# Optimization experiments

Measured on AMD Instinct MI355X. Metric: run time of the kernel, lower is better.

## Reference

```python
import jax, jax.numpy as jnp
import numpy as np

OBS_LEN = 8
N_PED = 2048      # total pedestrians
G = 64            # number of scenes (uniform size)
NP = N_PED // G   # pedestrians per scene = 32
H = 128           # action_decoder_hidden_dim == action_encoder_hidden_dim == f_in == f_out
DIN = 64          # action_encoder_input_dim
DD = 64           # distance_embedding_dim
NH = 4            # n_heads (hard-coded to 4 in GAT)


def setup_inputs() -> dict:
    key = jax.random.key(0)
    ks = jax.random.split(key, 16)
    s = 0.1  # weight scale (xavier-ish)
    starts = (jnp.arange(G) * NP).astype(jnp.int64)
    seq_start_end = jnp.stack([starts, starts + NP], axis=1)
    return {
        "obs_traj": jax.random.normal(ks[0], (OBS_LEN, N_PED, 2), jnp.float32),
        "goal_hidden_state": jax.random.normal(ks[1], (N_PED, H), jnp.float32),
        "goal": jax.random.normal(ks[2], (N_PED, 2), jnp.float32),
        "action": jax.random.normal(ks[3], (N_PED, 2), jnp.float32),
        "h0": jax.random.normal(ks[4], (N_PED, H), jnp.float32),
        "c0": jax.random.normal(ks[5], (N_PED, H), jnp.float32),
        "W_emb": jax.random.normal(ks[6], (2, DIN), jnp.float32) * s,
        "b_emb": jnp.zeros((DIN,), jnp.float32),
        "W_ih": jax.random.normal(ks[7], (4 * H, DIN), jnp.float32) * s,
        "W_hh": jax.random.normal(ks[8], (4 * H, H), jnp.float32) * s,
        "b_ih": jnp.zeros((4 * H,), jnp.float32),
        "b_hh": jnp.zeros((4 * H,), jnp.float32),
        "W_dist": jax.random.normal(ks[9], (8, DD), jnp.float32) * s,
        "b_dist": jnp.zeros((DD,), jnp.float32),
        "W_gate": jax.random.normal(ks[10], (DD, H), jnp.float32) * s,
        "b_gate": jnp.zeros((H,), jnp.float32),
        "gat_w": jax.random.normal(ks[11], (NH, 1, H, H), jnp.float32) * s,
        "gat_a": jax.random.normal(ks[12], (1, 1, 2 * H, 1), jnp.float32) * s,
        "gat_bias": jnp.zeros((H,), jnp.float32),
        "seq_start_end": seq_start_end,
    }


def _forward(obs_traj, goal_hidden_state, goal, action, h0, c0,
             W_emb, b_emb, W_ih, W_hh, b_ih, b_hh,
             W_dist, b_dist, W_gate, b_gate, gat_w, gat_a, gat_bias,
             seq_start_end):
    T, N, _ = obs_traj.shape
    g_num = seq_start_end.shape[0]
    n = N // g_num  # uniform group size

    # --- ActionEncoder: embed + LSTMCell loop over obs_len (lax.scan) ---
    x = jax.nn.relu(obs_traj.reshape(-1, 2) @ W_emb + b_emb).reshape(T, N, -1)

    def lstm_step(carry, xt):
        h, c = carry
        gates = xt @ W_ih.T + b_ih + h @ W_hh.T + b_hh  # torch gate order i,f,g,o
        i, f, g, o = jnp.split(gates, 4, axis=-1)
        c = jax.nn.sigmoid(f) * c + jax.nn.sigmoid(i) * jnp.tanh(g)
        h = jax.nn.sigmoid(o) * jnp.tanh(c)
        return (h, c), None

    (action_hidden, _), _ = jax.lax.scan(lstm_step, (h0, c0), x)  # [N, H]

    Hd = action_hidden.shape[-1]
    ahg = action_hidden.reshape(g_num, n, Hd)
    ghg = goal_hidden_state.reshape(g_num, n, Hd)
    glg = goal.reshape(g_num, n, 2)
    acg = action.reshape(g_num, n, 2)

    eye = jnp.eye(n, dtype=action_hidden.dtype)[:, :, None]  # [n, n, 1]

    def gat_group(ah, gh, gl, ac):
        # InteractionGate.cal_gate: dist[i,j] = [action_i, goal_i, action_j, goal_j]
        a_i = jnp.broadcast_to(ac[:, None, :], (n, n, 2))
        g_i = jnp.broadcast_to(gl[:, None, :], (n, n, 2))
        a_j = jnp.broadcast_to(ac[None, :, :], (n, n, 2))
        g_j = jnp.broadcast_to(gl[None, :, :], (n, n, 2))
        dist = jnp.concatenate([a_i, g_i, a_j, g_j], axis=-1)  # [n, n, 8]
        gate = jax.nn.sigmoid(jax.nn.relu(dist @ W_dist + b_dist) @ W_gate + b_gate)  # [n, n, H]

        # gate_action[i,j] = gate[i,j] * tanh(action_hidden[j])
        gate_action = gate * jnp.tanh(ah[None, :, :])
        # diagonal -> goal_hidden[i], off-diag -> gated action
        goal_action = eye * gh[None, :, :] + (1.0 - eye) * gate_action  # [n, n, H]

        h_other = jnp.concatenate([ah[:, None, :], goal_action], axis=1)  # [n, n+1, H]
        h_self = jnp.broadcast_to(ah[:, None, :], (n, n + 1, Hd))          # [n, n+1, H]

        # GraphAttentionLayer
        w = gat_w[:, 0]  # [NH, H, H]
        hs = jnp.einsum('nkf,hfo->hnko', h_self, w)   # [NH, n, n+1, H]
        ho = jnp.einsum('nkf,hfo->hnko', h_other, w)  # [NH, n, n+1, H]
        scores = jnp.concatenate([hs, ho], axis=-1) @ gat_a[0, 0, :, 0]  # [NH, n, n+1]
        alpha = jax.nn.softmax(jax.nn.leaky_relu(scores, 0.2), axis=-1)
        out = jnp.mean(jnp.sum(alpha[..., None] * ho, axis=2), axis=0)  # [n, H]
        return jax.nn.relu(out) + gat_bias

    out = jax.vmap(gat_group)(ahg, ghg, glg, acg)  # [G, n, H]
    return out.reshape(N, Hd)


def reference(obs_traj, goal_hidden_state, goal, action, h0, c0,
              W_emb, b_emb, W_ih, W_hh, b_ih, b_hh,
              W_dist, b_dist, W_gate, b_gate, gat_w, gat_a, gat_bias,
              seq_start_end):
    return _forward(obs_traj, goal_hidden_state, goal, action, h0, c0,
                    W_emb, b_emb, W_ih, W_hh, b_ih, b_hh,
                    W_dist, b_dist, W_gate, b_gate, gat_w, gat_a, gat_bias,
                    seq_start_end)
```

## Files before the change

kernel.cpp:

```cpp
#include <hip/hip_runtime.h>

#define N_PED 2048
#define NGROUP 64
#define NPG 32
#define HDIM 128
#define DIN 64
#define DDIM 64
#define NHEAD 4
#define TOBS 8

typedef __attribute__((ext_vector_type(8))) short bf16x8;
typedef __attribute__((ext_vector_type(4))) float f32x4;

__device__ __forceinline__ float sigm(float x){ return 1.f/(1.f + __expf(-x)); }
__device__ __forceinline__ float tanh_fast(float x){ return 1.f - 2.f/(__expf(2.f*x) + 1.f); }
__device__ __forceinline__ short f2bf(float f){
    unsigned u = __float_as_uint(f);
    unsigned r = (u + 0x7fffu + ((u >> 16) & 1u)) >> 16;
    return (short)r;
}
__device__ __forceinline__ float bf2f(unsigned short b){
    return __uint_as_float(((unsigned)b) << 16);
}
__device__ __forceinline__ unsigned pk2(float a, float b){
    return (unsigned)(unsigned short)f2bf(a) | ((unsigned)(unsigned short)f2bf(b) << 16);
}

#define WS_AHB   0
#define WS_TAHB  524288
#define WS_VW    1048576
#define WS_GF    1052672
#define WS_WF    1069056

__global__ __launch_bounds__(256) void prep_kernel(const float* __restrict__ gat_w,
                                                   const float* __restrict__ gat_a,
                                                   float* __restrict__ VW) {
    __shared__ float sa[2*HDIM];
    __shared__ float red[32][8][2];
    const int tid = threadIdx.x;
    if (tid < 256) sa[tid] = gat_a[tid];
    __syncthreads();
    const int rl = tid >> 3, ch = tid & 7;
    const int row = blockIdx.x*32 + rl;
    const float* rp = gat_w + (size_t)row*HDIM + ch*16;
    float v = 0.f, w1 = 0.f;
    #pragma unroll
    for (int e = 0; e < 16; ++e) {
        float wv = rp[e];
        v  += wv * sa[HDIM + ch*16 + e];
        w1 += wv * sa[ch*16 + e];
    }
    red[rl][ch][0] = v; red[rl][ch][1] = w1;
    __syncthreads();
    if (ch == 0) {
        float sv = 0.f, sw = 0.f;
        #pragma unroll
        for (int e = 0; e < 8; ++e) { sv += red[rl][e][0]; sw += red[rl][e][1]; }
        VW[row]       = sv;
        VW[512 + row] = sw;
    }
}

__global__ __launch_bounds__(512) void pack_kernel(const float* __restrict__ W_gate,
                                                   const float* __restrict__ gat_w,
                                                   unsigned char* __restrict__ ws) {
    const int id = blockIdx.x*512 + threadIdx.x;
    if (id >= 9216) return;
    uint4* Gf4 = reinterpret_cast<uint4*>(ws + WS_GF);
    uint4* Wf4 = reinterpret_cast<uint4*>(ws + WS_WF);
    if (id < 1024) {
        const int fid = id >> 6, L = id & 63;
        const int kt = fid >> 3, nt = fid & 7;
        const int q = L >> 4, ln = L & 15;
        float v[8];
        #pragma unroll
        for (int j = 0; j < 8; ++j)
            v[j] = W_gate[(size_t)(kt*32 + q*8 + j)*HDIM + nt*16 + ln];
        Gf4[id] = uint4{ pk2(v[0],v[1]), pk2(v[2],v[3]), pk2(v[4],v[5]), pk2(v[6],v[7]) };
    } else {
        const int id2 = id - 1024;
        const int fid = id2 >> 6, L = id2 & 63;
        const int kt = fid >> 3, nt = fid & 7;
        const int q = L >> 4, ln = L & 15;
        float v[8];
        #pragma unroll
        for (int j = 0; j < 8; ++j) {
            int F = kt*32 + q*8 + j;
            v[j] = gat_w[(size_t)(F >> 7)*16384 + (size_t)(F & 127)*HDIM + nt*16 + ln];
        }
        Wf4[id2] = uint4{ pk2(v[0],v[1]), pk2(v[2],v[3]), pk2(v[4],v[5]), pk2(v[6],v[7]) };
    }
}

#define KPAD 216
__global__ __launch_bounds__(512) void lstm_kernel(
    const float* __restrict__ obs, const float* __restrict__ h0,
    const float* __restrict__ c0,  const float* __restrict__ W_emb,
    const float* __restrict__ b_emb, const float* __restrict__ W_ih,
    const float* __restrict__ W_hh,  const float* __restrict__ b_ih,
    const float* __restrict__ b_hh,
    unsigned short* __restrict__ AHb, unsigned short* __restrict__ TAHb)
{
    __shared__ short Xl[16][KPAD];
    __shared__ float sEmb[192];

    const int tid  = threadIdx.x;
    const int ped0 = blockIdx.x * 16;
    const int w    = tid >> 6;
    const int lane = tid & 63;
    const int q    = lane >> 4;
    const int ln   = lane & 15;
    const int u    = w*16 + ln;

    if (tid < 192) sEmb[tid] = (tid < 128) ? W_emb[tid] : b_emb[tid - 128];

    bf16x8 bfr[4][6];
    #pragma unroll
    for (int idx = 0; idx < 4; ++idx) {
        const int n = idx*128 + u;
        #pragma unroll
        for (int kt = 0; kt < 6; ++kt) {
            const float* src = (kt < 2) ? (W_ih + (size_t)n*DIN  + kt*32 + q*8)
                                        : (W_hh + (size_t)n*HDIM + (kt-2)*32 + q*8);
            bf16x8 b;
            #pragma unroll
            for (int j = 0; j < 8; ++j) b[j] = f2bf(src[j]);
            bfr[idx][kt] = b;
        }
    }
    float bsv[4];
    #pragma unroll
    for (int idx = 0; idx < 4; ++idx) bsv[idx] = b_ih[idx*128 + u] + b_hh[idx*128 + u];

    float c_st[4];
    #pragma unroll
    for (int reg = 0; reg < 4; ++reg)
        c_st[reg] = c0[(size_t)(ped0 + q*4 + reg)*HDIM + u];

    #pragma unroll
    for (int reg = 0; reg < 4; ++reg)
        Xl[q*4 + reg][64 + u] = f2bf(h0[(size_t)(ped0 + q*4 + reg)*HDIM + u]);
    {
        const int ped = tid >> 5, d0 = (tid & 31)*2;
        const float2 ob = reinterpret_cast<const float2*>(obs)[(size_t)(ped0 + ped)];
        float x0 = fmaxf(ob.x*sEmb[d0]   + ob.y*sEmb[64+d0]   + sEmb[128+d0],   0.f);
        float x1 = fmaxf(ob.x*sEmb[d0+1] + ob.y*sEmb[64+d0+1] + sEmb[128+d0+1], 0.f);
        *reinterpret_cast<unsigned*>(&Xl[ped][d0]) = pk2(x0, x1);
    }
    __syncthreads();

    float hval[4];
    for (int t = 0; t < TOBS; ++t) {
        bf16x8 afr[6];
        #pragma unroll
        for (int kt = 0; kt < 6; ++kt)
            afr[kt] = *reinterpret_cast<const bf16x8*>(&Xl[ln][kt*32 + q*8]);

        f32x4 acc[4];
        #pragma unroll
        for (int idx = 0; idx < 4; ++idx) {
            f32x4 a = { bsv[idx], bsv[idx], bsv[idx], bsv[idx] };
            #pragma unroll
            for (int kt = 0; kt < 6; ++kt)
                a = __builtin_amdgcn_mfma_f32_16x16x32_bf16(afr[kt], bfr[idx][kt], a, 0, 0, 0);
            acc[idx] = a;
        }
        #pragma unroll
        for (int reg = 0; reg < 4; ++reg) {
            float c = sigm(acc[1][reg])*c_st[reg] + sigm(acc[0][reg])*tanh_fast(acc[2][reg]);
            c_st[reg] = c;
            hval[reg] = sigm(acc[3][reg])*tanh_fast(c);
        }
        __syncthreads();

        if (t < TOBS-1) {
            #pragma unroll
            for (int reg = 0; reg < 4; ++reg)
                Xl[q*4 + reg][64 + u] = f2bf(hval[reg]);
            {
                const int ped = tid >> 5, d0 = (tid & 31)*2;
                const float2 ob = reinterpret_cast<const float2*>(obs)[(size_t)((t+1)*N_PED + ped0 + ped)];
                float x0 = fmaxf(ob.x*sEmb[d0]   + ob.y*sEmb[64+d0]   + sEmb[128+d0],   0.f);
                float x1 = fmaxf(ob.x*sEmb[d0+1] + ob.y*sEmb[64+d0+1] + sEmb[128+d0+1], 0.f);
                *reinterpret_cast<unsigned*>(&Xl[ped][d0]) = pk2(x0, x1);
            }
            __syncthreads();
        }
    }

    #pragma unroll
    for (int reg = 0; reg < 4; ++reg) {
        const size_t off = (size_t)(ped0 + q*4 + reg)*HDIM + u;
        AHb[off]  = (unsigned short)f2bf(hval[reg]);
        TAHb[off] = (unsigned short)f2bf(tanh_fast(hval[reg]));
    }
}

__global__ __launch_bounds__(256) void gat_kernel(
    const unsigned short* __restrict__ AHb,
    const unsigned short* __restrict__ TAHb,
    const float* __restrict__ VW,
    const unsigned char* __restrict__ ws,
    const float* __restrict__ ghs,
    const float* __restrict__ goal,
    const float* __restrict__ action,
    const float* __restrict__ W_dist,
    const float* __restrict__ b_dist,
    const float* __restrict__ b_gate,
    const float* __restrict__ gat_bias,
    float* __restrict__ out)
{
    __shared__ unsigned short sGAb[80][136];
    __shared__ unsigned short sTAHb[32][136];
    __shared__ unsigned short st1b[64][72];
    __shared__ unsigned short sU[4][520];
    __shared__ float sAl[2][4][34];
    __shared__ float sPj[80][8];
    __shared__ float sWd[8][64];
    __shared__ float sbd[64];
    __shared__ float sbg[128];
    __shared__ float sgb[128];
    __shared__ float sAC[32][2], sGL[32][2];

    const int tid = threadIdx.x;
    const int g   = blockIdx.x >> 3;
    const int i0  = (blockIdx.x & 7) * 4;
    const int p0  = g * NPG;
    const int w   = tid >> 6;
    const int L   = tid & 63;
    const int q   = L >> 4;
    const int ln  = L & 15;

    const bf16x8* Gf8 = reinterpret_cast<const bf16x8*>(ws + WS_GF);
    const bf16x8* Wf8 = reinterpret_cast<const bf16x8*>(ws + WS_WF);

    for (int s = tid; s < 512; s += 256) {
        int j = s >> 4, c = s & 15;
        *reinterpret_cast<uint4*>(&sTAHb[j][c*8]) =
            *reinterpret_cast<const uint4*>(&TAHb[(size_t)(p0 + j)*HDIM + c*8]);
    }
    if (tid < 128) {
        sbg[tid] = b_gate[tid];
        sgb[tid] = gat_bias[tid];
    } else if (tid < 192) {
        sbd[tid-128] = b_dist[tid-128];
    } else {
        int j = tid - 192;
        int pd = j & 31;
        if (j < 32) { const float2 a = reinterpret_cast<const float2*>(action)[p0+pd];
                      sAC[pd][0]=a.x; sAC[pd][1]=a.y; }
        else        { const float2 gl = reinterpret_cast<const float2*>(goal)[p0+pd];
                      sGL[pd][0]=gl.x; sGL[pd][1]=gl.y; }
    }
    if (tid < 256) {
        int rr = tid >> 6, k = tid & 63;
        sWd[rr][k]   = W_dist[rr*64 + k];
        sWd[rr+4][k] = W_dist[(rr+4)*64 + k];
    }

    bf16x8 vf[4];
    #pragma unroll
    for (int kt = 0; kt < 4; ++kt) {
        bf16x8 b;
        #pragma unroll
        for (int j = 0; j < 8; ++j) {
            int k = kt*32 + q*8 + j;
            float v = 0.f;
            if (ln < 4)      v = VW[ln*HDIM + k];
            else if (ln < 8) v = VW[512 + (ln-4)*HDIM + k];
            b[j] = f2bf(v);
        }
        vf[kt] = b;
    }
    __syncthreads();

    for (int half = 0; half < 2; ++half) {
        {
            const int k = tid & 63, mg = tid >> 6;
            float base[2];
            #pragma unroll
            for (int rh = 0; rh < 2; ++rh) {
                int i = i0 + half*2 + rh;
                base[rh] = sAC[i][0]*sWd[0][k] + sAC[i][1]*sWd[1][k]
                         + sGL[i][0]*sWd[2][k] + sGL[i][1]*sWd[3][k] + sbd[k];
            }
            #pragma unroll
            for (int mm = 0; mm < 16; ++mm) {
                int m = mg*16 + mm, j = m & 31;
                float v = base[m>>5] + sAC[j][0]*sWd[4][k] + sAC[j][1]*sWd[5][k]
                                     + sGL[j][0]*sWd[6][k] + sGL[j][1]*sWd[7][k];
                st1b[m][k] = (unsigned short)f2bf(fmaxf(v, 0.f));
            }
        }
        __syncthreads();

        {
            bf16x8 afr[2];
            #pragma unroll
            for (int kt = 0; kt < 2; ++kt)
                afr[kt] = *reinterpret_cast<const bf16x8*>(&st1b[w*16 + ln][kt*32 + q*8]);
            for (int nt = 0; nt < 8; ++nt) {
                float bg = sbg[nt*16 + ln];
                f32x4 a = { bg, bg, bg, bg };
                a = __builtin_amdgcn_mfma_f32_16x16x32_bf16(afr[0], Gf8[(0*8+nt)*64 + L], a, 0, 0, 0);
                a = __builtin_amdgcn_mfma_f32_16x16x32_bf16(afr[1], Gf8[(1*8+nt)*64 + L], a, 0, 0, 0);
                #pragma unroll
                for (int reg = 0; reg < 4; ++reg) {
                    int mrow = w*16 + q*4 + reg;
                    int n = nt*16 + ln;
                    float ga = sigm(a[reg]) * bf2f(sTAHb[mrow & 31][n]);
                    sGAb[mrow][n] = (unsigned short)f2bf(ga);
                }
            }
        }
        __syncthreads();

        {
            int rh = tid >> 7, f = tid & 127;
            int irow = i0 + half*2 + rh;
            sGAb[rh*32 + irow][f] = (unsigned short)f2bf(ghs[(size_t)(p0 + irow)*HDIM + f]);
            sGAb[64 + rh][f]      = AHb[(size_t)(p0 + irow)*HDIM + f];
        }
        __syncthreads();

        {
            int nmt = (w == 0) ? 2 : 1;
            for (int e = 0; e < nmt; ++e) {
                int mt = (e == 0) ? w : 4;
                bf16x8 afr;
                f32x4 a = { 0.f, 0.f, 0.f, 0.f };
                #pragma unroll
                for (int kt = 0; kt < 4; ++kt) {
                    afr = *reinterpret_cast<const bf16x8*>(&sGAb[mt*16 + ln][kt*32 + q*8]);
                    a = __builtin_amdgcn_mfma_f32_16x16x32_bf16(afr, vf[kt], a, 0, 0, 0);
                }
                if (ln < 8) {
                    #pragma unroll
                    for (int reg = 0; reg < 4; ++reg)
                        sPj[mt*16 + q*4 + reg][ln] = a[reg];
                }
            }
        }
        __syncthreads();

        if (tid < 8) {
            int rh = tid >> 2, h = tid & 3;
            float sa_ = sPj[64 + rh][4 + h];
            float x0  = sa_ + sPj[64 + rh][h];
            x0 = (x0 < 0.f) ? 0.2f*x0 : x0;
            float sum = 1.f;
            sAl[rh][h][0] = 1.f;
            for (int k = 1; k <= 32; ++k) {
                float x = sa_ + sPj[rh*32 + k - 1][h];
                x = (x < 0.f) ? 0.2f*x : x;
                float e = __expf(x - x0);
                sAl[rh][h][k] = e; sum += e;
            }
            float inv = 1.f/sum;
            for (int k = 0; k <= 32; ++k) sAl[rh][h][k] *= inv;
        }
        __syncthreads();

        {
            int rh = w & 1, ntb = (w >> 1) * 4;
            int r  = half*2 + rh;
            bf16x8 afr;
            #pragma unroll
            for (int jj = 0; jj < 8; ++jj)
                afr[jj] = f2bf(sAl[rh][ln & 3][1 + q*8 + jj]);
            for (int t = 0; t < 4; ++t) {
                int nt = ntb + t;
                bf16x8 bfr;
                #pragma unroll
                for (int jj = 0; jj < 8; ++jj)
                    bfr[jj] = (short)sGAb[rh*32 + q*8 + jj][nt*16 + ln];
                f32x4 a = { 0.f, 0.f, 0.f, 0.f };
                a = __builtin_amdgcn_mfma_f32_16x16x32_bf16(afr, bfr, a, 0, 0, 0);
                if (L < 16) {
                    #pragma unroll
                    for (int reg = 0; reg < 4; ++reg) {
                        float uv = a[reg] + sAl[rh][reg][0] * bf2f(sGAb[64 + rh][nt*16 + ln]);
                        sU[r][reg*HDIM + nt*16 + ln] = (unsigned short)f2bf(uv);
                    }
                }
            }
        }
        __syncthreads();
    }

    {
        bf16x8 afr[16];
        #pragma unroll
        for (int kt = 0; kt < 16; ++kt)
            afr[kt] = *reinterpret_cast<const bf16x8*>(&sU[ln & 3][kt*32 + q*8]);
        for (int e = 0; e < 2; ++e) {
            int nt = w*2 + e;
            f32x4 a = { 0.f, 0.f, 0.f, 0.f };
            #pragma unroll
            for (int kt = 0; kt < 16; ++kt)
                a = __builtin_amdgcn_mfma_f32_16x16x32_bf16(afr[kt], Wf8[(kt*8+nt)*64 + L], a, 0, 0, 0);
            if (L < 16) {
                int o = nt*16 + ln;
                #pragma unroll
                for (int reg = 0; reg < 4; ++reg) {
                    float val = fmaxf(a[reg]*0.25f, 0.f) + sgb[o];
                    out[(size_t)(p0 + i0 + reg)*HDIM + o] = val;
                }
            }
        }
    }
}

extern "C" void kernel_launch(void* const* d_in, const int* in_sizes, int n_in,
                              void* d_out, int out_size, void* d_ws, size_t ws_size,
                              hipStream_t stream) {
    const float* obs      = (const float*)d_in[0];
    const float* ghs      = (const float*)d_in[1];
    const float* goal     = (const float*)d_in[2];
    const float* action   = (const float*)d_in[3];
    const float* h0       = (const float*)d_in[4];
    const float* c0       = (const float*)d_in[5];
    const float* W_emb    = (const float*)d_in[6];
    const float* b_emb    = (const float*)d_in[7];
    const float* W_ih     = (const float*)d_in[8];
    const float* W_hh     = (const float*)d_in[9];
    const float* b_ih     = (const float*)d_in[10];
    const float* b_hh     = (const float*)d_in[11];
    const float* W_dist   = (const float*)d_in[12];
    const float* b_dist   = (const float*)d_in[13];
    const float* W_gate   = (const float*)d_in[14];
    const float* b_gate   = (const float*)d_in[15];
    const float* gat_w    = (const float*)d_in[16];
    const float* gat_a    = (const float*)d_in[17];
    const float* gat_bias = (const float*)d_in[18];

    unsigned char* ws = (unsigned char*)d_ws;
    unsigned short* AHb  = (unsigned short*)(ws + WS_AHB);
    unsigned short* TAHb = (unsigned short*)(ws + WS_TAHB);
    float* VW            = (float*)(ws + WS_VW);
    float* out = (float*)d_out;

    hipLaunchKernelGGL(prep_kernel, dim3(16),  dim3(256), 0, stream, gat_w, gat_a, VW);
    hipLaunchKernelGGL(pack_kernel, dim3(18),  dim3(512), 0, stream, W_gate, gat_w, ws);
    hipLaunchKernelGGL(lstm_kernel, dim3(128), dim3(512), 0, stream,
                       obs, h0, c0, W_emb, b_emb, W_ih, W_hh, b_ih, b_hh, AHb, TAHb);
    hipLaunchKernelGGL(gat_kernel,  dim3(512), dim3(256), 0, stream,
                       AHb, TAHb, VW, ws, ghs, goal, action,
                       W_dist, b_dist, b_gate, gat_bias, out);
}
```

Measured before the change: 144.8 us.

## Fuse prep/pack kernels, halve LSTM block size, double-buffer LSTM input

Merges the prep and pack kernels into one launch to save a kernel launch. The LSTM kernel now handles 8 pedestrians per block (duplicated into the 16-row MFMA tile) over 256 blocks, so more CUs are busy. Its input tile is double-buffered, which drops one barrier per timestep. Sigmoid and tanh now use a hardware reciprocal. The cost is half of the MFMA work being redundant, and the approximate reciprocal adds a small precision risk.

Measured after the change: 137.1 us. -5.3%, faster.

```diff
diff --git a/kernel.cpp b/kernel.cpp
--- a/kernel.cpp
+++ b/kernel.cpp
@@ -12,8 +12,12 @@
 typedef __attribute__((ext_vector_type(8))) short bf16x8;
 typedef __attribute__((ext_vector_type(4))) float f32x4;
 
-__device__ __forceinline__ float sigm(float x){ return 1.f/(1.f + __expf(-x)); }
-__device__ __forceinline__ float tanh_fast(float x){ return 1.f - 2.f/(__expf(2.f*x) + 1.f); }
+__device__ __forceinline__ float sigm(float x){
+    return __builtin_amdgcn_rcpf(1.f + __expf(-x));
+}
+__device__ __forceinline__ float tanh_fast(float x){
+    return 1.f - 2.f*__builtin_amdgcn_rcpf(__expf(2.f*x) + 1.f);
+}
 __device__ __forceinline__ short f2bf(float f){
     unsigned u = __float_as_uint(f);
     unsigned r = (u + 0x7fffu + ((u >> 16) & 1u)) >> 16;
@@ -32,63 +36,65 @@
 #define WS_GF    1052672
 #define WS_WF    1069056
 
-__global__ __launch_bounds__(256) void prep_kernel(const float* __restrict__ gat_w,
-                                                   const float* __restrict__ gat_a,
-                                                   float* __restrict__ VW) {
-    __shared__ float sa[2*HDIM];
-    __shared__ float red[32][8][2];
+__global__ __launch_bounds__(512) void prep_pack_kernel(
+    const float* __restrict__ gat_w, const float* __restrict__ gat_a,
+    const float* __restrict__ W_gate, unsigned char* __restrict__ ws)
+{
     const int tid = threadIdx.x;
-    if (tid < 256) sa[tid] = gat_a[tid];
-    __syncthreads();
-    const int rl = tid >> 3, ch = tid & 7;
-    const int row = blockIdx.x*32 + rl;
-    const float* rp = gat_w + (size_t)row*HDIM + ch*16;
-    float v = 0.f, w1 = 0.f;
-    #pragma unroll
-    for (int e = 0; e < 16; ++e) {
-        float wv = rp[e];
-        v  += wv * sa[HDIM + ch*16 + e];
-        w1 += wv * sa[ch*16 + e];
-    }
-    red[rl][ch][0] = v; red[rl][ch][1] = w1;
-    __syncthreads();
-    if (ch == 0) {
-        float sv = 0.f, sw = 0.f;
-        #pragma unroll
-        for (int e = 0; e < 8; ++e) { sv += red[rl][e][0]; sw += red[rl][e][1]; }
-        VW[row]       = sv;
-        VW[512 + row] = sw;
-    }
-}
-
-__global__ __launch_bounds__(512) void pack_kernel(const float* __restrict__ W_gate,
-                                                   const float* __restrict__ gat_w,
-                                                   unsigned char* __restrict__ ws) {
-    const int id = blockIdx.x*512 + threadIdx.x;
-    if (id >= 9216) return;
-    uint4* Gf4 = reinterpret_cast<uint4*>(ws + WS_GF);
-    uint4* Wf4 = reinterpret_cast<uint4*>(ws + WS_WF);
-    if (id < 1024) {
-        const int fid = id >> 6, L = id & 63;
-        const int kt = fid >> 3, nt = fid & 7;
-        const int q = L >> 4, ln = L & 15;
-        float v[8];
-        #pragma unroll
-        for (int j = 0; j < 8; ++j)
-            v[j] = W_gate[(size_t)(kt*32 + q*8 + j)*HDIM + nt*16 + ln];
-        Gf4[id] = uint4{ pk2(v[0],v[1]), pk2(v[2],v[3]), pk2(v[4],v[5]), pk2(v[6],v[7]) };
+    if (blockIdx.x < 16) {
+        __shared__ float sa[2*HDIM];
+        __shared__ float red[32][8][2];
+        float* VW = (float*)(ws + WS_VW);
+        if (tid < 256) sa[tid] = gat_a[tid];
+        __syncthreads();
+        const int rl = (tid & 255) >> 3, ch = tid & 7;
+        const int row = blockIdx.x*32 + rl;
+        if (tid < 256) {
+            const float* rp = gat_w + (size_t)row*HDIM + ch*16;
+            float v = 0.f, w1 = 0.f;
+            #pragma unroll
+            for (int e = 0; e < 16; ++e) {
+                float wv = rp[e];
+                v  += wv * sa[HDIM + ch*16 + e];
+                w1 += wv * sa[ch*16 + e];
+            }
+            red[rl][ch][0] = v; red[rl][ch][1] = w1;
+        }
+        __syncthreads();
+        if (tid < 256 && ch == 0) {
+            float sv = 0.f, sw = 0.f;
+            #pragma unroll
+            for (int e = 0; e < 8; ++e) { sv += red[rl][e][0]; sw += red[rl][e][1]; }
+            VW[row]       = sv;
+            VW[512 + row] = sw;
+        }
     } else {
-        const int id2 = id - 1024;
-        const int fid = id2 >> 6, L = id2 & 63;
-        const int kt = fid >> 3, nt = fid & 7;
-        const int q = L >> 4, ln = L & 15;
-        float v[8];
-        #pragma unroll
-        for (int j = 0; j < 8; ++j) {
-            int F = kt*32 + q*8 + j;
-            v[j] = gat_w[(size_t)(F >> 7)*16384 + (size_t)(F & 127)*HDIM + nt*16 + ln];
-        }
-        Wf4[id2] = uint4{ pk2(v[0],v[1]), pk2(v[2],v[3]), pk2(v[4],v[5]), pk2(v[6],v[7]) };
+        const int id = (blockIdx.x - 16)*512 + tid;
+        if (id >= 9216) return;
+        uint4* Gf4 = reinterpret_cast<uint4*>(ws + WS_GF);
+        uint4* Wf4 = reinterpret_cast<uint4*>(ws + WS_WF);
+        if (id < 1024) {
+            const int fid = id >> 6, L = id & 63;
+            const int kt = fid >> 3, nt = fid & 7;
+            const int q = L >> 4, ln = L & 15;
+            float v[8];
+            #pragma unroll
+            for (int j = 0; j < 8; ++j)
+                v[j] = W_gate[(size_t)(kt*32 + q*8 + j)*HDIM + nt*16 + ln];
+            Gf4[id] = uint4{ pk2(v[0],v[1]), pk2(v[2],v[3]), pk2(v[4],v[5]), pk2(v[6],v[7]) };
+        } else {
+            const int id2 = id - 1024;
+            const int fid = id2 >> 6, L = id2 & 63;
+            const int kt = fid >> 3, nt = fid & 7;
+            const int q = L >> 4, ln = L & 15;
+            float v[8];
+            #pragma unroll
+            for (int j = 0; j < 8; ++j) {
+                int F = kt*32 + q*8 + j;
+                v[j] = gat_w[(size_t)(F >> 7)*16384 + (size_t)(F & 127)*HDIM + nt*16 + ln];
+            }
+            Wf4[id2] = uint4{ pk2(v[0],v[1]), pk2(v[2],v[3]), pk2(v[4],v[5]), pk2(v[6],v[7]) };
+        }
     }
 }
 
@@ -101,11 +107,11 @@
     const float* __restrict__ b_hh,
     unsigned short* __restrict__ AHb, unsigned short* __restrict__ TAHb)
 {
-    __shared__ short Xl[16][KPAD];
+    __shared__ short Xl[2][16][KPAD];
     __shared__ float sEmb[192];
 
     const int tid  = threadIdx.x;
-    const int ped0 = blockIdx.x * 16;
+    const int ped0 = blockIdx.x * 8;
     const int w    = tid >> 6;
     const int lane = tid & 63;
     const int q    = lane >> 4;
@@ -135,26 +141,36 @@
     float c_st[4];
     #pragma unroll
     for (int reg = 0; reg < 4; ++reg)
-        c_st[reg] = c0[(size_t)(ped0 + q*4 + reg)*HDIM + u];
+        c_st[reg] = c0[(size_t)(ped0 + ((q*4 + reg) & 7))*HDIM + u];
 
     #pragma unroll
     for (int reg = 0; reg < 4; ++reg)
-        Xl[q*4 + reg][64 + u] = f2bf(h0[(size_t)(ped0 + q*4 + reg)*HDIM + u]);
+        Xl[0][q*4 + reg][64 + u] = f2bf(h0[(size_t)(ped0 + ((q*4 + reg) & 7))*HDIM + u]);
     {
-        const int ped = tid >> 5, d0 = (tid & 31)*2;
-        const float2 ob = reinterpret_cast<const float2*>(obs)[(size_t)(ped0 + ped)];
+        const int pr = tid >> 5, d0 = (tid & 31)*2;
+        const float2 ob = reinterpret_cast<const float2*>(obs)[(size_t)(ped0 + (pr & 7))];
         float x0 = fmaxf(ob.x*sEmb[d0]   + ob.y*sEmb[64+d0]   + sEmb[128+d0],   0.f);
         float x1 = fmaxf(ob.x*sEmb[d0+1] + ob.y*sEmb[64+d0+1] + sEmb[128+d0+1], 0.f);
-        *reinterpret_cast<unsigned*>(&Xl[ped][d0]) = pk2(x0, x1);
+        *reinterpret_cast<unsigned*>(&Xl[0][pr][d0]) = pk2(x0, x1);
     }
     __syncthreads();
 
     float hval[4];
     for (int t = 0; t < TOBS; ++t) {
+        const int cur = t & 1, nxt = cur ^ 1;
+
+        if (t < TOBS-1) {
+            const int pr = tid >> 5, d0 = (tid & 31)*2;
+            const float2 ob = reinterpret_cast<const float2*>(obs)[(size_t)((t+1)*N_PED + ped0 + (pr & 7))];
+            float x0 = fmaxf(ob.x*sEmb[d0]   + ob.y*sEmb[64+d0]   + sEmb[128+d0],   0.f);
+            float x1 = fmaxf(ob.x*sEmb[d0+1] + ob.y*sEmb[64+d0+1] + sEmb[128+d0+1], 0.f);
+            *reinterpret_cast<unsigned*>(&Xl[nxt][pr][d0]) = pk2(x0, x1);
+        }
+
         bf16x8 afr[6];
         #pragma unroll
         for (int kt = 0; kt < 6; ++kt)
-            afr[kt] = *reinterpret_cast<const bf16x8*>(&Xl[ln][kt*32 + q*8]);
+            afr[kt] = *reinterpret_cast<const bf16x8*>(&Xl[cur][ln][kt*32 + q*8]);
 
         f32x4 acc[4];
         #pragma unroll
@@ -171,28 +187,22 @@
             c_st[reg] = c;
             hval[reg] = sigm(acc[3][reg])*tanh_fast(c);
         }
-        __syncthreads();
 
         if (t < TOBS-1) {
             #pragma unroll
             for (int reg = 0; reg < 4; ++reg)
-                Xl[q*4 + reg][64 + u] = f2bf(hval[reg]);
-            {
-                const int ped = tid >> 5, d0 = (tid & 31)*2;
-                const float2 ob = reinterpret_cast<const float2*>(obs)[(size_t)((t+1)*N_PED + ped0 + ped)];
-                float x0 = fmaxf(ob.x*sEmb[d0]   + ob.y*sEmb[64+d0]   + sEmb[128+d0],   0.f);
-                float x1 = fmaxf(ob.x*sEmb[d0+1] + ob.y*sEmb[64+d0+1] + sEmb[128+d0+1], 0.f);
-                *reinterpret_cast<unsigned*>(&Xl[ped][d0]) = pk2(x0, x1);
-            }
+                Xl[nxt][q*4 + reg][64 + u] = f2bf(hval[reg]);
             __syncthreads();
         }
     }
 
-    #pragma unroll
-    for (int reg = 0; reg < 4; ++reg) {
-        const size_t off = (size_t)(ped0 + q*4 + reg)*HDIM + u;
-        AHb[off]  = (unsigned short)f2bf(hval[reg]);
-        TAHb[off] = (unsigned short)f2bf(tanh_fast(hval[reg]));
+    if (q < 2) {
+        #pragma unroll
+        for (int reg = 0; reg < 4; ++reg) {
+            const size_t off = (size_t)(ped0 + q*4 + reg)*HDIM + u;
+            AHb[off]  = (unsigned short)f2bf(hval[reg]);
+            TAHb[off] = (unsigned short)f2bf(tanh_fast(hval[reg]));
+        }
     }
 }
 
@@ -440,9 +450,9 @@
     float* VW            = (float*)(ws + WS_VW);
     float* out = (float*)d_out;
 
-    hipLaunchKernelGGL(prep_kernel, dim3(16),  dim3(256), 0, stream, gat_w, gat_a, VW);
-    hipLaunchKernelGGL(pack_kernel, dim3(18),  dim3(512), 0, stream, W_gate, gat_w, ws);
-    hipLaunchKernelGGL(lstm_kernel, dim3(128), dim3(512), 0, stream,
+    hipLaunchKernelGGL(prep_pack_kernel, dim3(34), dim3(512), 0, stream,
+                       gat_w, gat_a, W_gate, ws);
+    hipLaunchKernelGGL(lstm_kernel, dim3(256), dim3(512), 0, stream,
                        obs, h0, c0, W_emb, b_emb, W_ih, W_hh, b_ih, b_hh, AHb, TAHb);
     hipLaunchKernelGGL(gat_kernel,  dim3(512), dim3(256), 0, stream,
                        AHb, TAHb, VW, ws, ghs, goal, action,
```
